# Kernel tuning notes

Hardware: AMD Instinct MI355X
Metric: run time of the kernel (lower is better)

## Reference

```python
import jax, jax.numpy as jnp
import numpy as np

B, N, D, NS, HID = 64, 4096, 256, 8, 512
ITERS = 3
EPS = 1e-08
SCALE = D ** -0.5
LN_EPS = 1e-5


def _layernorm(x, g, b):
    m = x.mean(-1, keepdims=True)
    v = ((x - m) ** 2).mean(-1, keepdims=True)
    return (x - m) * jax.lax.rsqrt(v + LN_EPS) * g + b


def setup_inputs() -> dict:
    key = jax.random.key(0)
    ks = jax.random.split(key, 20)
    s = 0.02
    return {
        "inputs": jax.random.normal(ks[0], (B, N, D), jnp.float32),
        "noise": jax.random.normal(ks[1], (B, NS, D), jnp.float32),
        "slots_mu": jax.random.normal(ks[2], (1, 1, D), jnp.float32),
        "slots_logsigma": jax.random.normal(ks[3], (1, 1, D), jnp.float32) * s,
        "Wq": jax.random.normal(ks[4], (D, D), jnp.float32) * s,  # (in, out): y = x @ Wq
        "Wk": jax.random.normal(ks[5], (D, D), jnp.float32) * s,
        "Wv": jax.random.normal(ks[6], (D, D), jnp.float32) * s,
        "gru_wi": jax.random.normal(ks[7], (3 * D, D), jnp.float32) * s,  # torch GRUCell weight_ih
        "gru_wh": jax.random.normal(ks[8], (3 * D, D), jnp.float32) * s,
        "gru_bi": jnp.zeros((3 * D,), jnp.float32),
        "gru_bh": jnp.zeros((3 * D,), jnp.float32),
        "mlp_w1": jax.random.normal(ks[9], (D, HID), jnp.float32) * s,
        "mlp_b1": jnp.zeros((HID,), jnp.float32),
        "mlp_w2": jax.random.normal(ks[10], (HID, D), jnp.float32) * s,
        "mlp_b2": jnp.zeros((D,), jnp.float32),
        "ln_in_g": jnp.ones((D,), jnp.float32),
        "ln_in_b": jnp.zeros((D,), jnp.float32),
        "ln_s_g": jnp.ones((D,), jnp.float32),
        "ln_s_b": jnp.zeros((D,), jnp.float32),
        "ln_ff_g": jnp.ones((D,), jnp.float32),
        "ln_ff_b": jnp.zeros((D,), jnp.float32),
    }


def _step(slots, k, v, Wq, gru_wi, gru_wh, gru_bi, gru_bh,
          mlp_w1, mlp_b1, mlp_w2, mlp_b2, ln_s_g, ln_s_b, ln_ff_g, ln_ff_b):
    b, ns, d = slots.shape
    slots_prev = slots
    q = _layernorm(slots, ln_s_g, ln_s_b) @ Wq                  # [b, ns, d]
    dots = jnp.einsum('bid,bjd->bij', q, k) * SCALE             # [b, ns, n]
    attn = jax.nn.softmax(dots, axis=1) + EPS                   # softmax over slot dim
    attn = attn / attn.sum(-1, keepdims=True)                   # renormalize over tokens
    updates = jnp.einsum('bjd,bij->bid', v, attn)               # [b, ns, d]
    # GRUCell (torch semantics)
    x = updates.reshape(-1, d)
    h = slots_prev.reshape(-1, d)
    gi = x @ gru_wi.T + gru_bi
    gh = h @ gru_wh.T + gru_bh
    ir, iz, inn = jnp.split(gi, 3, axis=-1)
    hr, hz, hn = jnp.split(gh, 3, axis=-1)
    r = jax.nn.sigmoid(ir + hr)
    z = jax.nn.sigmoid(iz + hz)
    nng = jnp.tanh(inn + r * hn)
    h_new = (1.0 - z) * nng + z * h
    slots = h_new.reshape(b, ns, d)
    ff = _layernorm(slots, ln_ff_g, ln_ff_b)
    slots = slots + jax.nn.relu(ff @ mlp_w1 + mlp_b1) @ mlp_w2 + mlp_b2
    return slots


def reference(inputs, noise, slots_mu, slots_logsigma, Wq, Wk, Wv,
              gru_wi, gru_wh, gru_bi, gru_bh,
              mlp_w1, mlp_b1, mlp_w2, mlp_b2,
              ln_in_g, ln_in_b, ln_s_g, ln_s_b, ln_ff_g, ln_ff_b):
    slots = slots_mu + jnp.exp(slots_logsigma) * noise          # [B, NS, D]
    x = _layernorm(inputs, ln_in_g, ln_in_b)
    k = x @ Wk
    v = x @ Wv
    args = (Wq, gru_wi, gru_wh, gru_bi, gru_bh, mlp_w1, mlp_b1, mlp_w2, mlp_b2,
            ln_s_g, ln_s_b, ln_ff_g, ln_ff_b)
    for _ in range(ITERS):
        slots = _step(slots, k, v, *args)
    slots = _step(jax.lax.stop_gradient(slots), k, v, *args)
    return slots
```

## Files before the change

kernel.cpp:

```cpp
#include <hip/hip_runtime.h>
#include <cstdint>

#define B_ 64
#define N_ 4096
#define D_ 256
#define NS_ 8
#define HID_ 512
#define TOK_ 128
#define NPART_ 32
#define EPS_ 1e-8f
#define SCALE_ 0.0625f
#define LN_EPS_ 1e-5f

typedef _Float16 f16;
typedef __attribute__((ext_vector_type(4))) _Float16 f16x4;
typedef __attribute__((ext_vector_type(8))) _Float16 f16x8;
typedef __attribute__((ext_vector_type(4))) float f32x4;

#define MFMA16(a, b, c) __builtin_amdgcn_mfma_f32_16x16x32_f16(a, b, c, 0, 0, 0)

__global__ __launch_bounds__(256) void k_setup(
    const float* __restrict__ in, const float* __restrict__ gin,
    const float* __restrict__ bin, f16* __restrict__ xh,
    const float* __restrict__ Wk, float* __restrict__ WkX,
    const float* __restrict__ wi, const float* __restrict__ wh,
    f16* __restrict__ wiTh, f16* __restrict__ whTh,
    const float* __restrict__ noise, const float* __restrict__ mu,
    const float* __restrict__ ls, float* __restrict__ slots,
    const float* __restrict__ w1, const float* __restrict__ w2,
    f16* __restrict__ w1h, f16* __restrict__ w2h) {
  const int blk = blockIdx.x;
  const int t = threadIdx.x;
  if (blk < 65536) {
    const int wave = t >> 6, lane = t & 63;
    const size_t row = (size_t)blk * 4 + wave;
    const float* r = in + row * D_;
    float4 a = *(const float4*)(r + lane * 4);
    float s1 = a.x + a.y + a.z + a.w;
    float s2 = a.x * a.x + a.y * a.y + a.z * a.z + a.w * a.w;
    #pragma unroll
    for (int m = 32; m >= 1; m >>= 1) { s1 += __shfl_xor(s1, m, 64); s2 += __shfl_xor(s2, m, 64); }
    const float mean = s1 * (1.f / D_);
    const float rstd = rsqrtf(s2 * (1.f / D_) - mean * mean + LN_EPS_);
    float4 gg = *(const float4*)(gin + lane * 4);
    float4 bv = *(const float4*)(bin + lane * 4);
    f16x4 o;
    o[0] = (f16)((a.x - mean) * rstd * gg.x + bv.x);
    o[1] = (f16)((a.y - mean) * rstd * gg.y + bv.y);
    o[2] = (f16)((a.z - mean) * rstd * gg.z + bv.z);
    o[3] = (f16)((a.w - mean) * rstd * gg.w + bv.w);
    *(f16x4*)(xh + row * D_ + lane * 4) = o;
  } else if (blk < 65792) {
    const int e = blk - 65536;
    WkX[t * 256 + e] = Wk[e * 256 + t];
  } else if (blk < 66560) {
    const int idx = (blk - 65792) * 256 + t;
    const int o = idx >> 8, d = idx & 255;
    wiTh[d * 768 + o] = (f16)wi[idx];
    whTh[d * 768 + o] = (f16)wh[idx];
  } else if (blk < 67072) {
    const int idx = (blk - 66560) * 256 + t;
    const int d = idx & 255;
    slots[idx] = mu[d] + __expf(ls[d]) * noise[idx];
  } else if (blk < 67584) {
    const int idx = (blk - 67072) * 256 + t;
    w1h[idx] = (f16)w1[idx];
  } else {
    const int idx = (blk - 67584) * 256 + t;
    w2h[idx] = (f16)w2[idx];
  }
}

__global__ __launch_bounds__(256) void k_m(const float* __restrict__ Wq,
                                           const float* __restrict__ WkX,
                                           float* __restrict__ M) {
  __shared__ float wq[256];
  const int c = blockIdx.x, e = threadIdx.x;
  wq[e] = Wq[c * 256 + e];
  __syncthreads();
  float a0 = 0.f, a1 = 0.f, a2 = 0.f, a3 = 0.f;
  #pragma unroll 8
  for (int d = 0; d < 256; d += 4) {
    a0 = fmaf(wq[d],     WkX[(d)     * 256 + e], a0);
    a1 = fmaf(wq[d + 1], WkX[(d + 1) * 256 + e], a1);
    a2 = fmaf(wq[d + 2], WkX[(d + 2) * 256 + e], a2);
    a3 = fmaf(wq[d + 3], WkX[(d + 3) * 256 + e], a3);
  }
  M[c * 256 + e] = (a0 + a1 + a2 + a3) * SCALE_;
}

__global__ __launch_bounds__(256) void k_qk(const float* __restrict__ slots,
    const float* __restrict__ g, const float* __restrict__ b,
    const float* __restrict__ M, f16* __restrict__ qkh) {
  const int row = blockIdx.x;
  const int t = threadIdx.x;
  __shared__ float sl[256];
  __shared__ float red1[4], red2[4];
  float val = slots[(size_t)row * D_ + t];
  float s1 = val, s2 = val * val;
  #pragma unroll
  for (int m = 32; m >= 1; m >>= 1) { s1 += __shfl_xor(s1, m, 64); s2 += __shfl_xor(s2, m, 64); }
  int wave = t >> 6, lane = t & 63;
  if (lane == 0) { red1[wave] = s1; red2[wave] = s2; }
  __syncthreads();
  s1 = red1[0] + red1[1] + red1[2] + red1[3];
  s2 = red2[0] + red2[1] + red2[2] + red2[3];
  float mean = s1 * (1.f / D_);
  float rstd = rsqrtf(s2 * (1.f / D_) - mean * mean + LN_EPS_);
  sl[t] = (val - mean) * rstd * g[t] + b[t];
  __syncthreads();
  float a0 = 0.f, a1 = 0.f, a2 = 0.f, a3 = 0.f;
  #pragma unroll 8
  for (int d = 0; d < D_; d += 4) {
    a0 = fmaf(sl[d],     M[(d)     * D_ + t], a0);
    a1 = fmaf(sl[d + 1], M[(d + 1) * D_ + t], a1);
    a2 = fmaf(sl[d + 2], M[(d + 2) * D_ + t], a2);
    a3 = fmaf(sl[d + 3], M[(d + 3) * D_ + t], a3);
  }
  qkh[((size_t)(row >> 3) * 16 + (row & 7)) * D_ + t] = (f16)(a0 + a1 + a2 + a3);
}

__global__ __launch_bounds__(256) void k_attn_upd(
    const f16* __restrict__ xh, const f16* __restrict__ qkh,
    float* __restrict__ urp, float* __restrict__ asp) {
  __shared__ __align__(16) f16 xt[TOK_ * 256];
  __shared__ __align__(16) f16 qs[16 * 256];
  __shared__ float wv_s[TOK_ * 12];
  const int b = blockIdx.y;
  const int blkx = blockIdx.x;
  const int jt = blkx * TOK_;
  const int part = b * NPART_ + blkx;
  const int tid = threadIdx.x;
  const int wave = tid >> 6, lane = tid & 63;

  {
    const int r = tid >> 4, c0 = (tid & 15) * 2;
    const f16* src = qkh + ((size_t)b * 16 + r) * D_;
    *(f16x8*)&qs[r * 256 + ((c0)     ^ (r & 7)) * 8] = *(const f16x8*)(src + c0 * 8);
    *(f16x8*)&qs[r * 256 + ((c0 + 1) ^ (r & 7)) * 8] = *(const f16x8*)(src + c0 * 8 + 8);
  }
  {
    const f16* src = xh + ((size_t)b * N_ + jt) * D_;
    f16x8 v[16];
    #pragma unroll
    for (int i = 0; i < 16; ++i) {
      const int r = i * 8 + (tid >> 5), c = tid & 31;
      v[i] = *(const f16x8*)(src + r * 256 + c * 8);
    }
    #pragma unroll
    for (int i = 0; i < 16; ++i) {
      const int r = i * 8 + (tid >> 5), c = tid & 31;
      *(f16x8*)&xt[r * 256 + (c ^ (r & 7)) * 8] = v[i];
    }
  }
  __syncthreads();

  const int kg = lane >> 4;
  f16x8 afr[8];
  {
    const int arow = lane & 15;
    #pragma unroll
    for (int kk = 0; kk < 8; ++kk)
      afr[kk] = *(const f16x8*)&qs[arow * 256 + ((kk * 4 + kg) ^ (arow & 7)) * 8];
  }
  #pragma unroll
  for (int t2 = 0; t2 < 2; ++t2) {
    const int nt = wave * 2 + t2;
    const int tok = nt * 16 + (lane & 15);
    f32x4 acc = {0.f, 0.f, 0.f, 0.f};
    #pragma unroll
    for (int kk = 0; kk < 8; ++kk) {
      f16x8 bf = *(const f16x8*)&xt[tok * 256 + ((kk * 4 + kg) ^ (tok & 7)) * 8];
      acc = MFMA16(afr[kk], bf, acc);
    }
    float o0 = __shfl_xor(acc[0], 16, 64);
    float o1 = __shfl_xor(acc[1], 16, 64);
    float o2 = __shfl_xor(acc[2], 16, 64);
    float o3 = __shfl_xor(acc[3], 16, 64);
    if (lane < 32) {
      float m = fmaxf(fmaxf(fmaxf(acc[0], acc[1]), fmaxf(acc[2], acc[3])),
                      fmaxf(fmaxf(o0, o1), fmaxf(o2, o3)));
      float e0 = __expf(acc[0] - m), e1 = __expf(acc[1] - m);
      float e2 = __expf(acc[2] - m), e3 = __expf(acc[3] - m);
      float sm = e0 + e1 + e2 + e3;
      float so = __shfl_xor(sm, 16, 64);
      float inv = 1.f / (sm + so);
      float4 wv;
      wv.x = e0 * inv + EPS_; wv.y = e1 * inv + EPS_;
      wv.z = e2 * inv + EPS_; wv.w = e3 * inv + EPS_;
      *(float4*)&wv_s[tok * 12 + (lane >> 4) * 4] = wv;
    }
  }
  __syncthreads();

  {
    const int i0 = wave * 2;
    const int ch0 = lane >> 1, sub = (lane & 1) * 4;
    float a0[4] = {0.f, 0.f, 0.f, 0.f};
    float a1[4] = {0.f, 0.f, 0.f, 0.f};
    float s0 = 0.f, s1 = 0.f;
    #pragma unroll 4
    for (int j = 0; j < TOK_; ++j) {
      f16x4 v = *(const f16x4*)&xt[j * 256 + (ch0 ^ (j & 7)) * 8 + sub];
      float vx = (float)v[0], vy = (float)v[1], vz = (float)v[2], vw = (float)v[3];
      float w0 = wv_s[j * 12 + i0];
      float w1 = wv_s[j * 12 + i0 + 1];
      s0 += w0; s1 += w1;
      a0[0] = fmaf(w0, vx, a0[0]); a0[1] = fmaf(w0, vy, a0[1]);
      a0[2] = fmaf(w0, vz, a0[2]); a0[3] = fmaf(w0, vw, a0[3]);
      a1[0] = fmaf(w1, vx, a1[0]); a1[1] = fmaf(w1, vy, a1[1]);
      a1[2] = fmaf(w1, vz, a1[2]); a1[3] = fmaf(w1, vw, a1[3]);
    }
    float* u0 = urp + ((size_t)part * NS_ + i0) * D_ + lane * 4;
    *(float4*)(u0)      = make_float4(a0[0], a0[1], a0[2], a0[3]);
    *(float4*)(u0 + D_) = make_float4(a1[0], a1[1], a1[2], a1[3]);
    if (lane == 0) {
      asp[part * NS_ + i0]     = s0;
      asp[part * NS_ + i0 + 1] = s1;
    }
  }
}

__global__ __launch_bounds__(256) void k_gru_mlp(
    const float* __restrict__ urp, const float* __restrict__ asp,
    const float* __restrict__ slots, const float* __restrict__ Wv,
    const f16* __restrict__ wiTh, const f16* __restrict__ whTh,
    const float* __restrict__ bi, const float* __restrict__ bh,
    const f16* __restrict__ w1h, const float* __restrict__ b1,
    const f16* __restrict__ w2h, const float* __restrict__ b2,
    const float* __restrict__ gf, const float* __restrict__ bf,
    const float* __restrict__ gs, const float* __restrict__ bs,
    const float* __restrict__ M,
    float* __restrict__ out, f16* __restrict__ qkh) {
  const int row = blockIdx.x;
  const int bb = row >> 3, ii = row & 7;
  const int t = threadIdx.x;
  __shared__ float urs[256], xs[256], hs[256], ffs[256], hid[512];
  __shared__ float red1[4], red2[4];
  const int wave = t >> 6, lane = t & 63;
  const float hv = slots[(size_t)row * D_ + t];
  hs[t] = hv;
  {
    float usum = 0.f;
    #pragma unroll 8
    for (int p = 0; p < NPART_; ++p)
      usum += urp[((size_t)(bb * NPART_ + p) * NS_ + ii) * D_ + t];
    urs[t] = usum;
  }
  {
    float ap = (t < NPART_) ? asp[(size_t)(bb * NPART_ + t) * NS_ + ii] : 0.f;
    #pragma unroll
    for (int m = 16; m >= 1; m >>= 1) ap += __shfl_xor(ap, m, 64);
    if (t == 0) red1[0] = ap;
  }
  __syncthreads();
  const float asv = red1[0];
  {
    const float ia = 1.f / asv;
    float u0 = 0.f, u1 = 0.f, u2 = 0.f, u3 = 0.f;
    #pragma unroll 8
    for (int e = 0; e < D_; e += 4) {
      u0 = fmaf(urs[e],     Wv[(size_t)(e)     * D_ + t], u0);
      u1 = fmaf(urs[e + 1], Wv[(size_t)(e + 1) * D_ + t], u1);
      u2 = fmaf(urs[e + 2], Wv[(size_t)(e + 2) * D_ + t], u2);
      u3 = fmaf(urs[e + 3], Wv[(size_t)(e + 3) * D_ + t], u3);
    }
    xs[t] = (u0 + u1 + u2 + u3) * ia;
  }
  __syncthreads();
  float gi0 = bi[t], gi1 = bi[D_ + t], gi2 = bi[2 * D_ + t];
  float gh0 = bh[t], gh1 = bh[D_ + t], gh2 = bh[2 * D_ + t];
  #pragma unroll 8
  for (int d = 0; d < D_; ++d) {
    const f16* wid = wiTh + d * 768;
    const f16* whd = whTh + d * 768;
    float xd = xs[d], hd = hs[d];
    gi0 = fmaf(xd, (float)wid[t], gi0);
    gi1 = fmaf(xd, (float)wid[D_ + t], gi1);
    gi2 = fmaf(xd, (float)wid[2 * D_ + t], gi2);
    gh0 = fmaf(hd, (float)whd[t], gh0);
    gh1 = fmaf(hd, (float)whd[D_ + t], gh1);
    gh2 = fmaf(hd, (float)whd[2 * D_ + t], gh2);
  }
  float r = 1.f / (1.f + __expf(-(gi0 + gh0)));
  float z = 1.f / (1.f + __expf(-(gi1 + gh1)));
  float n = tanhf(gi2 + r * gh2);
  float hnew = (1.f - z) * n + z * hv;
  float s1 = hnew, s2 = hnew * hnew;
  #pragma unroll
  for (int m = 32; m >= 1; m >>= 1) { s1 += __shfl_xor(s1, m, 64); s2 += __shfl_xor(s2, m, 64); }
  if (lane == 0) { red1[wave] = s1; red2[wave] = s2; }
  __syncthreads();
  s1 = red1[0] + red1[1] + red1[2] + red1[3];
  s2 = red2[0] + red2[1] + red2[2] + red2[3];
  float mean = s1 * (1.f / D_);
  float rstd = rsqrtf(s2 * (1.f / D_) - mean * mean + LN_EPS_);
  ffs[t] = (hnew - mean) * rstd * gf[t] + bf[t];
  __syncthreads();
  {
    float h1a = b1[t], h2a = b1[D_ + t], h1b = 0.f, h2b = 0.f;
    #pragma unroll 8
    for (int d = 0; d < D_; d += 2) {
      float f0 = ffs[d], f1 = ffs[d + 1];
      h1a = fmaf(f0, (float)w1h[(size_t)(d)     * HID_ + t],      h1a);
      h2a = fmaf(f0, (float)w1h[(size_t)(d)     * HID_ + D_ + t], h2a);
      h1b = fmaf(f1, (float)w1h[(size_t)(d + 1) * HID_ + t],      h1b);
      h2b = fmaf(f1, (float)w1h[(size_t)(d + 1) * HID_ + D_ + t], h2b);
    }
    hid[t] = fmaxf(h1a + h1b, 0.f); hid[D_ + t] = fmaxf(h2a + h2b, 0.f);
  }
  __syncthreads();
  float o;
  {
    float oa = b2[t], ob = 0.f;
    #pragma unroll 8
    for (int d = 0; d < HID_; d += 2) {
      oa = fmaf(hid[d],     (float)w2h[(size_t)(d)     * D_ + t], oa);
      ob = fmaf(hid[d + 1], (float)w2h[(size_t)(d + 1) * D_ + t], ob);
    }
    o = oa + ob + hnew;
  }
  out[(size_t)row * D_ + t] = o;
  s1 = o; s2 = o * o;
  #pragma unroll
  for (int m = 32; m >= 1; m >>= 1) { s1 += __shfl_xor(s1, m, 64); s2 += __shfl_xor(s2, m, 64); }
  __syncthreads();
  if (lane == 0) { red1[wave] = s1; red2[wave] = s2; }
  __syncthreads();
  s1 = red1[0] + red1[1] + red1[2] + red1[3];
  s2 = red2[0] + red2[1] + red2[2] + red2[3];
  mean = s1 * (1.f / D_);
  rstd = rsqrtf(s2 * (1.f / D_) - mean * mean + LN_EPS_);
  ffs[t] = (o - mean) * rstd * gs[t] + bs[t];
  __syncthreads();
  {
    float a0 = 0.f, a1 = 0.f, a2 = 0.f, a3 = 0.f;
    #pragma unroll 8
    for (int d = 0; d < D_; d += 4) {
      a0 = fmaf(ffs[d],     M[(d)     * D_ + t], a0);
      a1 = fmaf(ffs[d + 1], M[(d + 1) * D_ + t], a1);
      a2 = fmaf(ffs[d + 2], M[(d + 2) * D_ + t], a2);
      a3 = fmaf(ffs[d + 3], M[(d + 3) * D_ + t], a3);
    }
    qkh[((size_t)(row >> 3) * 16 + (row & 7)) * D_ + t] = (f16)(a0 + a1 + a2 + a3);
  }
}

extern "C" void kernel_launch(void* const* d_in, const int* in_sizes, int n_in,
                              void* d_out, int out_size, void* d_ws, size_t ws_size,
                              hipStream_t stream) {
  (void)in_sizes; (void)n_in; (void)out_size; (void)ws_size;
  const float* inputs = (const float*)d_in[0];
  const float* noise  = (const float*)d_in[1];
  const float* mu     = (const float*)d_in[2];
  const float* ls     = (const float*)d_in[3];
  const float* Wq     = (const float*)d_in[4];
  const float* Wk     = (const float*)d_in[5];
  const float* Wv     = (const float*)d_in[6];
  const float* gwi    = (const float*)d_in[7];
  const float* gwh    = (const float*)d_in[8];
  const float* gbi    = (const float*)d_in[9];
  const float* gbh    = (const float*)d_in[10];
  const float* w1     = (const float*)d_in[11];
  const float* b1     = (const float*)d_in[12];
  const float* w2     = (const float*)d_in[13];
  const float* b2     = (const float*)d_in[14];
  const float* gin    = (const float*)d_in[15];
  const float* bin    = (const float*)d_in[16];
  const float* gs     = (const float*)d_in[17];
  const float* bs     = (const float*)d_in[18];
  const float* gff    = (const float*)d_in[19];
  const float* bff    = (const float*)d_in[20];

  const size_t KV = (size_t)B_ * N_ * D_;
  f16*   xh    = (f16*)d_ws;
  float* slots = (float*)(xh + KV);
  f16*   qkh   = (f16*)(slots + 131072);
  float* asp   = (float*)(qkh + 262144);
  float* urp   = asp + 16384;
  float* WkX   = urp + (size_t)B_ * NPART_ * NS_ * D_;
  float* M     = WkX + 65536;
  f16*   wiTh  = (f16*)(M + 65536);
  f16*   whTh  = wiTh + 196608;
  f16*   w1h   = whTh + 196608;
  f16*   w2h   = w1h + 131072;

  k_setup<<<68096, 256, 0, stream>>>(inputs, gin, bin, xh, Wk, WkX,
                                     gwi, gwh, wiTh, whTh,
                                     noise, mu, ls, slots, w1, w2, w1h, w2h);
  k_m<<<256, 256, 0, stream>>>(Wq, WkX, M);
  k_qk<<<512, 256, 0, stream>>>(slots, gs, bs, M, qkh);
  for (int it = 0; it < 4; ++it) {
    k_attn_upd<<<dim3(NPART_, B_), 256, 0, stream>>>(xh, qkh, urp, asp);
    float* outp = (it == 3) ? (float*)d_out : slots;
    k_gru_mlp<<<512, 256, 0, stream>>>(urp, asp, slots, Wv, wiTh, whTh, gbi, gbh,
                                       w1h, b1, w2h, b2, gff, bff, gs, bs, M,
                                       outp, qkh);
  }
}
```

Baseline: 488.2 us.

## Split attention-update accumulation over tokens per wave with shared-memory atomic reduction

```diff
diff --git a/kernel.cpp b/kernel.cpp
--- a/kernel.cpp
+++ b/kernel.cpp
@@ -126,6 +126,8 @@
   __shared__ __align__(16) f16 xt[TOK_ * 256];
   __shared__ __align__(16) f16 qs[16 * 256];
   __shared__ float wv_s[TOK_ * 12];
+  __shared__ float as_acc[NS_];
+  float* u_acc = (float*)qs;
   const int b = blockIdx.y;
   const int blkx = blockIdx.x;
   const int jt = blkx * TOK_;
@@ -193,31 +195,55 @@
   }
   __syncthreads();
 
-  {
-    const int i0 = wave * 2;
+  #pragma unroll
+  for (int c = 0; c < 8; ++c) u_acc[tid * 8 + c] = 0.f;
+  if (tid < NS_) as_acc[tid] = 0.f;
+  __syncthreads();
+
+  {
     const int ch0 = lane >> 1, sub = (lane & 1) * 4;
-    float a0[4] = {0.f, 0.f, 0.f, 0.f};
-    float a1[4] = {0.f, 0.f, 0.f, 0.f};
-    float s0 = 0.f, s1 = 0.f;
+    const int j0 = wave * 32;
+    float acc[8][4] = {};
+    float ssum[8] = {};
     #pragma unroll 4
-    for (int j = 0; j < TOK_; ++j) {
+    for (int jj = 0; jj < 32; ++jj) {
+      const int j = j0 + jj;
       f16x4 v = *(const f16x4*)&xt[j * 256 + (ch0 ^ (j & 7)) * 8 + sub];
       float vx = (float)v[0], vy = (float)v[1], vz = (float)v[2], vw = (float)v[3];
-      float w0 = wv_s[j * 12 + i0];
-      float w1 = wv_s[j * 12 + i0 + 1];
-      s0 += w0; s1 += w1;
-      a0[0] = fmaf(w0, vx, a0[0]); a0[1] = fmaf(w0, vy, a0[1]);
-      a0[2] = fmaf(w0, vz, a0[2]); a0[3] = fmaf(w0, vw, a0[3]);
-      a1[0] = fmaf(w1, vx, a1[0]); a1[1] = fmaf(w1, vy, a1[1]);
-      a1[2] = fmaf(w1, vz, a1[2]); a1[3] = fmaf(w1, vw, a1[3]);
-    }
-    float* u0 = urp + ((size_t)part * NS_ + i0) * D_ + lane * 4;
-    *(float4*)(u0)      = make_float4(a0[0], a0[1], a0[2], a0[3]);
-    *(float4*)(u0 + D_) = make_float4(a1[0], a1[1], a1[2], a1[3]);
+      const float* wr = &wv_s[j * 12];
+      float4 wA = *(const float4*)(wr);
+      float4 wB = *(const float4*)(wr + 4);
+      float w[8] = {wA.x, wA.y, wA.z, wA.w, wB.x, wB.y, wB.z, wB.w};
+      #pragma unroll
+      for (int i = 0; i < 8; ++i) {
+        ssum[i] += w[i];
+        acc[i][0] = fmaf(w[i], vx, acc[i][0]);
+        acc[i][1] = fmaf(w[i], vy, acc[i][1]);
+        acc[i][2] = fmaf(w[i], vz, acc[i][2]);
+        acc[i][3] = fmaf(w[i], vw, acc[i][3]);
+      }
+    }
+    const int dbase = lane * 4;
+    #pragma unroll
+    for (int i = 0; i < 8; ++i) {
+      atomicAdd(&u_acc[i * 256 + dbase + 0], acc[i][0]);
+      atomicAdd(&u_acc[i * 256 + dbase + 1], acc[i][1]);
+      atomicAdd(&u_acc[i * 256 + dbase + 2], acc[i][2]);
+      atomicAdd(&u_acc[i * 256 + dbase + 3], acc[i][3]);
+    }
     if (lane == 0) {
-      asp[part * NS_ + i0]     = s0;
-      asp[part * NS_ + i0 + 1] = s1;
-    }
+      #pragma unroll
+      for (int i = 0; i < 8; ++i) atomicAdd(&as_acc[i], ssum[i]);
+    }
+  }
+  __syncthreads();
+
+  {
+    const int s = tid >> 5, d0 = (tid & 31) * 8;
+    float* up = urp + ((size_t)part * NS_ + s) * D_ + d0;
+    *(float4*)(up)     = *(float4*)&u_acc[s * 256 + d0];
+    *(float4*)(up + 4) = *(float4*)&u_acc[s * 256 + d0 + 4];
+    if (tid < NS_) asp[part * NS_ + tid] = as_acc[tid];
   }
 }
 
```

New measurement: 778.1 us. 59.4% more time.
